# Kernel tuning notes

Measured on AMD Instinct MI355X. Metric: run time of the kernel, lower is better.

## Reference

```python
import jax, jax.numpy as jnp
import numpy as np

B, S, D, H = 4, 2048, 1024, 16
HD = D // H
MASK_VAL = -1e6  # d2l masked_softmax fill value


def setup_inputs() -> dict:
    key = jax.random.key(0)
    ks = jax.random.split(key, 8)
    scale = 1.0 / np.sqrt(D)
    return {
        "queries": jax.random.normal(ks[0], (B, S, D), dtype=jnp.float32),
        "keys": jax.random.normal(ks[1], (B, S, D), dtype=jnp.float32),
        "values": jax.random.normal(ks[2], (B, S, D), dtype=jnp.float32),
        "valid_lens": jax.random.randint(ks[3], (B,), 1, S + 1, dtype=jnp.int32),
        "Wq": jax.random.normal(ks[4], (D, D), dtype=jnp.float32) * scale,
        "Wk": jax.random.normal(ks[5], (D, D), dtype=jnp.float32) * scale,
        "Wv": jax.random.normal(ks[6], (D, D), dtype=jnp.float32) * scale,
        "Wo": jax.random.normal(ks[7], (D, D), dtype=jnp.float32) * scale,
    }


def reference(queries, keys, values, valid_lens, Wq, Wk, Wv, Wo):
    # QKV projections (no bias), then split into heads: [B,S,D] -> [B,H,S,HD]
    def split_heads(x):
        return x.reshape(B, S, H, HD).transpose(0, 2, 1, 3)

    q = split_heads(queries @ Wq)
    k = split_heads(keys @ Wk)
    v = split_heads(values @ Wv)

    # scaled dot-product scores: [B,H,Sq,Sk]
    scores = jnp.einsum('bhqd,bhkd->bhqk', q, k) / jnp.sqrt(jnp.float32(HD))

    # masked softmax over key axis: positions >= valid_len get -1e6 (d2l semantics)
    kv_pos = jnp.arange(S)  # [S]
    mask = kv_pos[None, :] < valid_lens[:, None]  # [B,S]
    scores = jnp.where(mask[:, None, None, :], scores, MASK_VAL)
    attn = jax.nn.softmax(scores, axis=-1)  # dropout=0.0 -> identity

    # weighted sum and merge heads: [B,H,S,HD] -> [B,S,D]
    out = jnp.einsum('bhqk,bhkd->bhqd', attn, v)
    out = out.transpose(0, 2, 1, 3).reshape(B, S, D)
    return out @ Wo
```

## Files before the change

### kernel.cpp

```cpp
#include <hip/hip_runtime.h>
#include <hip/hip_bf16.h>
#include <cstdint>
#include <cstddef>


typedef __hip_bfloat16 bf16;
typedef unsigned short u16;
typedef __attribute__((ext_vector_type(8))) unsigned short ushort8_t;
typedef __attribute__((ext_vector_type(8))) __bf16 bf16x8;
typedef __attribute__((ext_vector_type(4))) float f32x4;

constexpr int Bn = 4, Sn = 2048, Dn = 1024, Hn = 16, HDn = 64;
constexpr size_t BSD = (size_t)Bn * Sn * Dn;
constexpr size_t DD  = (size_t)Dn * Dn;

__device__ __forceinline__ u16 f2b(float f) {
    union { bf16 h; u16 u; } c; c.h = __float2bfloat16(f); return c.u;
}
__device__ __forceinline__ ushort8_t cvt8(float4 a, float4 b) {
    ushort8_t r;
    r[0] = f2b(a.x); r[1] = f2b(a.y); r[2] = f2b(a.z); r[3] = f2b(a.w);
    r[4] = f2b(b.x); r[5] = f2b(b.y); r[6] = f2b(b.z); r[7] = f2b(b.w);
    return r;
}

__global__ __launch_bounds__(256) void transpose_w(
    const float* __restrict__ S0, const float* __restrict__ S1, const float* __restrict__ S2,
    u16* __restrict__ D0, u16* __restrict__ D1, u16* __restrict__ D2)
{
    __shared__ u16 tl[32][33];
    const int z = blockIdx.z;
    const float* S = (z == 0) ? S0 : ((z == 1) ? S1 : S2);
    u16*         D = (z == 0) ? D0 : ((z == 1) ? D1 : D2);
    const int k0 = blockIdx.y * 32, n0 = blockIdx.x * 32;
    const int t = threadIdx.x;
    const int r = t >> 3, c0 = (t & 7) * 4;
    float4 v = *(const float4*)(S + (size_t)(k0 + r) * Dn + n0 + c0);
    tl[r][c0] = f2b(v.x); tl[r][c0 + 1] = f2b(v.y);
    tl[r][c0 + 2] = f2b(v.z); tl[r][c0 + 3] = f2b(v.w);
    __syncthreads();
    ushort4 o;
    o.x = tl[c0][r]; o.y = tl[c0 + 1][r]; o.z = tl[c0 + 2][r]; o.w = tl[c0 + 3][r];
    *(ushort4*)(D + (size_t)(n0 + r) * Dn + k0 + c0) = o;
}

__global__ __launch_bounds__(256) void gemm_qkv(
    const float* __restrict__ A0, const float* __restrict__ A1, const float* __restrict__ A2,
    const u16* __restrict__ B0, const u16* __restrict__ B1, const u16* __restrict__ B2,
    u16* __restrict__ C0, u16* __restrict__ C1, u16* __restrict__ C2, float qscale)
{
    constexpr int K = Dn, BK = 32, BM = 128;
    const int z = blockIdx.z;
    const float* A  = (z == 0) ? A0 : ((z == 1) ? A1 : A2);
    const u16*   Bt = (z == 0) ? B0 : ((z == 1) ? B1 : B2);
    u16*         C  = (z == 0) ? C0 : ((z == 1) ? C1 : C2);
    const float scale = (z == 0) ? qscale : 1.0f;

    __shared__ __attribute__((aligned(16))) u16 As[BM][BK + 8];
    __shared__ __attribute__((aligned(16))) u16 Bs[BM][BK + 8];

    const int t = threadIdx.x, l = t & 63, w = t >> 6;
    const int i = l & 15, j = l >> 4;
    const int row0 = blockIdx.y * BM, col0 = blockIdx.x * BM;
    const int m_off = (w & 1) * 64, n_off = (w >> 1) * 64;
    const int ar = t >> 1, ah = (t & 1) * 16;

    f32x4 acc[4][4] = {};

    for (int k0 = 0; k0 < K; k0 += BK) {
        const float* ap = A + (size_t)(row0 + ar) * K + k0 + ah;
        float4 f0 = *(const float4*)ap,       f1 = *(const float4*)(ap + 4);
        float4 f2 = *(const float4*)(ap + 8), f3 = *(const float4*)(ap + 12);
        const u16* bp = Bt + (size_t)(col0 + ar) * K + k0 + ah;
        ushort8_t bv0 = *(const ushort8_t*)bp, bv1 = *(const ushort8_t*)(bp + 8);
        __syncthreads();
        *(ushort8_t*)&As[ar][ah]     = cvt8(f0, f1);
        *(ushort8_t*)&As[ar][ah + 8] = cvt8(f2, f3);
        *(ushort8_t*)&Bs[ar][ah] = bv0; *(ushort8_t*)&Bs[ar][ah + 8] = bv1;
        __syncthreads();
        bf16x8 af[4], bfr[4];
        #pragma unroll
        for (int mi = 0; mi < 4; mi++)
            af[mi] = *(const bf16x8*)&As[m_off + mi * 16 + i][j * 8];
        #pragma unroll
        for (int ni = 0; ni < 4; ni++)
            bfr[ni] = *(const bf16x8*)&Bs[n_off + ni * 16 + i][j * 8];
        #pragma unroll
        for (int mi = 0; mi < 4; mi++)
            #pragma unroll
            for (int ni = 0; ni < 4; ni++)
                acc[mi][ni] = __builtin_amdgcn_mfma_f32_16x16x32_bf16(
                    af[mi], bfr[ni], acc[mi][ni], 0, 0, 0);
    }

    #pragma unroll
    for (int mi = 0; mi < 4; mi++) {
        #pragma unroll
        for (int r = 0; r < 4; r++) {
            const int m = row0 + m_off + mi * 16 + j * 4 + r;
            const int b = m >> 11, s = m & (Sn - 1);
            #pragma unroll
            for (int ni = 0; ni < 4; ni++) {
                const int n = col0 + n_off + ni * 16 + i;
                const int h = n >> 6, hd = n & (HDn - 1);
                C[(((size_t)(b * Hn + h)) * Sn + s) * HDn + hd] = f2b(acc[mi][ni][r] * scale);
            }
        }
    }
}

__global__ __launch_bounds__(256) void gemm_out(
    const u16* __restrict__ A, const u16* __restrict__ Bt, float* __restrict__ C)
{
    constexpr int K = Dn, BK = 32, BM = 128;
    __shared__ __attribute__((aligned(16))) u16 As[BM][BK + 8];
    __shared__ __attribute__((aligned(16))) u16 Bs[BM][BK + 8];

    const int t = threadIdx.x, l = t & 63, w = t >> 6;
    const int i = l & 15, j = l >> 4;
    const int row0 = blockIdx.y * BM, col0 = blockIdx.x * BM;
    const int m_off = (w & 1) * 64, n_off = (w >> 1) * 64;
    const int ar = t >> 1, ah = (t & 1) * 16;

    f32x4 acc[4][4] = {};

    for (int k0 = 0; k0 < K; k0 += BK) {
        const u16* ap = A  + (size_t)(row0 + ar) * K + k0 + ah;
        const u16* bp = Bt + (size_t)(col0 + ar) * K + k0 + ah;
        ushort8_t av0 = *(const ushort8_t*)ap, av1 = *(const ushort8_t*)(ap + 8);
        ushort8_t bv0 = *(const ushort8_t*)bp, bv1 = *(const ushort8_t*)(bp + 8);
        __syncthreads();
        *(ushort8_t*)&As[ar][ah] = av0; *(ushort8_t*)&As[ar][ah + 8] = av1;
        *(ushort8_t*)&Bs[ar][ah] = bv0; *(ushort8_t*)&Bs[ar][ah + 8] = bv1;
        __syncthreads();
        bf16x8 af[4], bfr[4];
        #pragma unroll
        for (int mi = 0; mi < 4; mi++)
            af[mi] = *(const bf16x8*)&As[m_off + mi * 16 + i][j * 8];
        #pragma unroll
        for (int ni = 0; ni < 4; ni++)
            bfr[ni] = *(const bf16x8*)&Bs[n_off + ni * 16 + i][j * 8];
        #pragma unroll
        for (int mi = 0; mi < 4; mi++)
            #pragma unroll
            for (int ni = 0; ni < 4; ni++)
                acc[mi][ni] = __builtin_amdgcn_mfma_f32_16x16x32_bf16(
                    af[mi], bfr[ni], acc[mi][ni], 0, 0, 0);
    }

    #pragma unroll
    for (int mi = 0; mi < 4; mi++) {
        #pragma unroll
        for (int r = 0; r < 4; r++) {
            const int m = row0 + m_off + mi * 16 + j * 4 + r;
            #pragma unroll
            for (int ni = 0; ni < 4; ni++) {
                const int n = col0 + n_off + ni * 16 + i;
                C[(size_t)m * Dn + n] = acc[mi][ni][r];
            }
        }
    }
}

__global__ __launch_bounds__(512) void attn_mfma(
    const u16* __restrict__ Qh, const u16* __restrict__ Kh, const u16* __restrict__ Vh,
    const int* __restrict__ vlen, u16* __restrict__ Out)
{
    constexpr int TQ = 128, TK = 64;
    __shared__ __attribute__((aligned(16))) u16 Ks[TK][HDn + 8];
    __shared__ __attribute__((aligned(16))) u16 Vt[HDn][TK + 8];
    __shared__ __attribute__((aligned(16))) u16 Ps[TQ][TK + 8];

    const int t = threadIdx.x, l = t & 63, w = t >> 6;
    const int i = l & 15, j = l >> 4;

    const int b    = blockIdx.x & 3;
    const int rest = blockIdx.x >> 2;
    const int h    = rest & 15;
    const int qt   = rest >> 4;
    const int q0   = qt * TQ;
    const int vl   = vlen[b];

    const size_t hoff = ((size_t)(b * Hn + h)) * Sn * HDn;
    const u16* Qg = Qh + hoff + (size_t)q0 * HDn;
    const u16* Kg = Kh + hoff;
    const u16* Vg = Vh + hoff;

    bf16x8 qf[2];
    #pragma unroll
    for (int ks = 0; ks < 2; ks++)
        qf[ks] = *(const bf16x8*)(Qg + (size_t)(w * 16 + i) * HDn + ks * 32 + j * 8);

    f32x4 acc_o[4] = {};
    float l_part[4] = {0.f, 0.f, 0.f, 0.f};

    const int ntiles = (vl + TK - 1) / TK;

    for (int kt = 0; kt < ntiles; kt++) {
        const int ks0 = kt * TK;
        __syncthreads();
        {
            const int kr = t >> 3, kc = (t & 7) * 8;
            *(ushort8_t*)&Ks[kr][kc] =
                *(const ushort8_t*)(Kg + (size_t)(ks0 + kr) * HDn + kc);
        }
        {
            const int vr = (t >> 4) * 2, dc = (t & 15) * 4;
            ushort4 v0 = *(const ushort4*)(Vg + (size_t)(ks0 + vr) * HDn + dc);
            ushort4 v1 = *(const ushort4*)(Vg + (size_t)(ks0 + vr + 1) * HDn + dc);
            *(ushort2*)&Vt[dc + 0][vr] = make_ushort2(v0.x, v1.x);
            *(ushort2*)&Vt[dc + 1][vr] = make_ushort2(v0.y, v1.y);
            *(ushort2*)&Vt[dc + 2][vr] = make_ushort2(v0.z, v1.z);
            *(ushort2*)&Vt[dc + 3][vr] = make_ushort2(v0.w, v1.w);
        }
        __syncthreads();

        f32x4 s[4] = {};
        #pragma unroll
        for (int ks = 0; ks < 2; ks++) {
            bf16x8 kf[4];
            #pragma unroll
            for (int ni = 0; ni < 4; ni++)
                kf[ni] = *(const bf16x8*)&Ks[ni * 16 + i][ks * 32 + j * 8];
            #pragma unroll
            for (int ni = 0; ni < 4; ni++)
                s[ni] = __builtin_amdgcn_mfma_f32_16x16x32_bf16(
                    qf[ks], kf[ni], s[ni], 0, 0, 0);
        }

        const bool tail = (ks0 + TK > vl);
        #pragma unroll
        for (int ni = 0; ni < 4; ni++) {
            const bool keep = !tail || (ks0 + ni * 16 + i < vl);
            #pragma unroll
            for (int r = 0; r < 4; r++) {
                float p = __expf(s[ni][r]);
                p = keep ? p : 0.0f;
                l_part[r] += p;
                Ps[w * 16 + j * 4 + r][ni * 16 + i] = f2b(p);
            }
        }

        #pragma unroll
        for (int ks = 0; ks < 2; ks++) {
            bf16x8 pa = *(const bf16x8*)&Ps[w * 16 + i][ks * 32 + j * 8];
            bf16x8 vb[4];
            #pragma unroll
            for (int di = 0; di < 4; di++)
                vb[di] = *(const bf16x8*)&Vt[di * 16 + i][ks * 32 + j * 8];
            #pragma unroll
            for (int di = 0; di < 4; di++)
                acc_o[di] = __builtin_amdgcn_mfma_f32_16x16x32_bf16(
                    pa, vb[di], acc_o[di], 0, 0, 0);
        }
    }

    #pragma unroll
    for (int r = 0; r < 4; r++) {
        float v = l_part[r];
        #pragma unroll
        for (int d = 1; d < 16; d <<= 1) v += __shfl_xor(v, d, 64);
        l_part[r] = v;
    }

    #pragma unroll
    for (int r = 0; r < 4; r++) {
        const int q = q0 + w * 16 + j * 4 + r;
        const float inv = 1.0f / l_part[r];
        #pragma unroll
        for (int di = 0; di < 4; di++) {
            const int d = di * 16 + i;
            Out[((size_t)b * Sn + q) * Dn + h * HDn + d] = f2b(acc_o[di][r] * inv);
        }
    }
}

extern "C" void kernel_launch(void* const* d_in, const int* in_sizes, int n_in,
                              void* d_out, int out_size, void* d_ws, size_t ws_size,
                              hipStream_t stream)
{
    const float* xq = (const float*)d_in[0];
    const float* xk = (const float*)d_in[1];
    const float* xv = (const float*)d_in[2];
    const int*   vl = (const int*)d_in[3];
    const float* Wq = (const float*)d_in[4];
    const float* Wk = (const float*)d_in[5];
    const float* Wv = (const float*)d_in[6];
    const float* Wo = (const float*)d_in[7];
    float* out = (float*)d_out;

    u16* Qh = (u16*)d_ws;
    u16* Kh = Qh + BSD;
    u16* Vh = Kh + BSD;
    u16* Ao = Vh + BSD;
    u16* WtQ = Ao;
    u16* WtK = WtQ + DD;
    u16* WtV = WtK + DD;
    u16* WoT = Qh;

    transpose_w<<<dim3(32, 32, 3), 256, 0, stream>>>(Wq, Wk, Wv, WtQ, WtK, WtV);
    gemm_qkv<<<dim3(8, 64, 3), 256, 0, stream>>>(xq, xk, xv, WtQ, WtK, WtV,
                                                 Qh, Kh, Vh, 0.125f);
    attn_mfma<<<dim3(Bn * Hn * (Sn / 128)), 512, 0, stream>>>(Qh, Kh, Vh, vl, Ao);
    transpose_w<<<dim3(32, 32, 1), 256, 0, stream>>>(Wo, Wo, Wo, WoT, WoT, WoT);
    gemm_out<<<dim3(8, 64), 256, 0, stream>>>(Ao, WoT, out);
}
```

Baseline: 412.3 us.

## Load GEMM tiles directly into LDS via global_load_lds with swizzle and tile remap

Both projection GEMMs now use the global_load_lds builtin to copy A and B tiles straight from global memory into shared memory, skipping the register round-trip. In the QKV GEMM the A tile is kept as fp32 in LDS with an XOR swizzle, and the bf16 conversion moves to fragment-read time. Block indices are also remapped so that consecutive blocks share row panels, which should improve L2 reuse. The padding on the LDS tiles is dropped, so B-tile fragment reads may suffer bank conflicts, and fp32 staging doubles the LDS footprint for A.

```diff
diff --git a/kernel.cpp b/kernel.cpp
--- a/kernel.cpp
+++ b/kernel.cpp
@@ -17,11 +17,18 @@
 __device__ __forceinline__ u16 f2b(float f) {
     union { bf16 h; u16 u; } c; c.h = __float2bfloat16(f); return c.u;
 }
-__device__ __forceinline__ ushort8_t cvt8(float4 a, float4 b) {
-    ushort8_t r;
-    r[0] = f2b(a.x); r[1] = f2b(a.y); r[2] = f2b(a.z); r[3] = f2b(a.w);
-    r[4] = f2b(b.x); r[5] = f2b(b.y); r[6] = f2b(b.z); r[7] = f2b(b.w);
-    return r;
+
+__device__ __forceinline__ bf16x8 cvt_bf8(f32x4 lo, f32x4 hi) {
+    union { ushort8_t u; bf16x8 b; } c;
+    c.u[0] = f2b(lo[0]); c.u[1] = f2b(lo[1]); c.u[2] = f2b(lo[2]); c.u[3] = f2b(lo[3]);
+    c.u[4] = f2b(hi[0]); c.u[5] = f2b(hi[1]); c.u[6] = f2b(hi[2]); c.u[7] = f2b(hi[3]);
+    return c.b;
+}
+
+__device__ __forceinline__ void gl_lds16(const void* g, void* l) {
+    __builtin_amdgcn_global_load_lds(
+        (const __attribute__((address_space(1))) uint32_t*)g,
+        (__attribute__((address_space(3))) uint32_t*)l, 16, 0, 0);
 }
 
 __global__ __launch_bounds__(256) void transpose_w(
@@ -56,32 +63,45 @@
     u16*         C  = (z == 0) ? C0 : ((z == 1) ? C1 : C2);
     const float scale = (z == 0) ? qscale : 1.0f;
 
-    __shared__ __attribute__((aligned(16))) u16 As[BM][BK + 8];
-    __shared__ __attribute__((aligned(16))) u16 Bs[BM][BK + 8];
+    __shared__ __attribute__((aligned(16))) float As32[BM][BK];
+    __shared__ __attribute__((aligned(16))) u16   Bs[BM][BK];
 
     const int t = threadIdx.x, l = t & 63, w = t >> 6;
     const int i = l & 15, j = l >> 4;
-    const int row0 = blockIdx.y * BM, col0 = blockIdx.x * BM;
+
+    const int wl   = blockIdx.x * 64 + blockIdx.y;
+    const int col0 = (wl & 7) * BM;
+    const int row0 = (wl >> 3) * BM;
     const int m_off = (w & 1) * 64, n_off = (w >> 1) * 64;
-    const int ar = t >> 1, ah = (t & 1) * 16;
+
+    const size_t a_base = (size_t)(row0 + w * 32 + (l >> 3)) * K
+                          + (size_t)(((l & 7) ^ (l >> 3)) * 4);
+    const size_t b_base = (size_t)(col0 + w * 32 + (l >> 2)) * K
+                          + (size_t)((l & 3) * 8);
+    float* a_lds = &As32[w * 32][0];
+    u16*   b_lds = &Bs[w * 32][0];
 
     f32x4 acc[4][4] = {};
 
     for (int k0 = 0; k0 < K; k0 += BK) {
-        const float* ap = A + (size_t)(row0 + ar) * K + k0 + ah;
-        float4 f0 = *(const float4*)ap,       f1 = *(const float4*)(ap + 4);
-        float4 f2 = *(const float4*)(ap + 8), f3 = *(const float4*)(ap + 12);
-        const u16* bp = Bt + (size_t)(col0 + ar) * K + k0 + ah;
-        ushort8_t bv0 = *(const ushort8_t*)bp, bv1 = *(const ushort8_t*)(bp + 8);
-        __syncthreads();
-        *(ushort8_t*)&As[ar][ah]     = cvt8(f0, f1);
-        *(ushort8_t*)&As[ar][ah + 8] = cvt8(f2, f3);
-        *(ushort8_t*)&Bs[ar][ah] = bv0; *(ushort8_t*)&Bs[ar][ah + 8] = bv1;
-        __syncthreads();
+        __syncthreads();
+        #pragma unroll
+        for (int c = 0; c < 4; c++)
+            gl_lds16(A + a_base + (size_t)c * 8 * K + k0, a_lds + c * 8 * BK);
+        #pragma unroll
+        for (int c = 0; c < 2; c++)
+            gl_lds16(Bt + b_base + (size_t)c * 16 * K + k0, b_lds + c * 16 * BK);
+        __syncthreads();
+
         bf16x8 af[4], bfr[4];
-        #pragma unroll
-        for (int mi = 0; mi < 4; mi++)
-            af[mi] = *(const bf16x8*)&As[m_off + mi * 16 + i][j * 8];
+        const int xa = i & 7;
+        #pragma unroll
+        for (int mi = 0; mi < 4; mi++) {
+            const float* rp = &As32[m_off + mi * 16 + i][0];
+            f32x4 lo = *(const f32x4*)(rp + ((2 * j)     ^ xa) * 4);
+            f32x4 hi = *(const f32x4*)(rp + ((2 * j + 1) ^ xa) * 4);
+            af[mi] = cvt_bf8(lo, hi);
+        }
         #pragma unroll
         for (int ni = 0; ni < 4; ni++)
             bfr[ni] = *(const bf16x8*)&Bs[n_off + ni * 16 + i][j * 8];
@@ -113,26 +133,33 @@
     const u16* __restrict__ A, const u16* __restrict__ Bt, float* __restrict__ C)
 {
     constexpr int K = Dn, BK = 32, BM = 128;
-    __shared__ __attribute__((aligned(16))) u16 As[BM][BK + 8];
-    __shared__ __attribute__((aligned(16))) u16 Bs[BM][BK + 8];
+    __shared__ __attribute__((aligned(16))) u16 As[BM][BK];
+    __shared__ __attribute__((aligned(16))) u16 Bs[BM][BK];
 
     const int t = threadIdx.x, l = t & 63, w = t >> 6;
     const int i = l & 15, j = l >> 4;
-    const int row0 = blockIdx.y * BM, col0 = blockIdx.x * BM;
+    const int wl   = blockIdx.x * 64 + blockIdx.y;
+    const int col0 = (wl & 7) * BM;
+    const int row0 = (wl >> 3) * BM;
     const int m_off = (w & 1) * 64, n_off = (w >> 1) * 64;
-    const int ar = t >> 1, ah = (t & 1) * 16;
+
+    const size_t a_base = (size_t)(row0 + w * 32 + (l >> 2)) * K + (size_t)((l & 3) * 8);
+    const size_t b_base = (size_t)(col0 + w * 32 + (l >> 2)) * K + (size_t)((l & 3) * 8);
+    u16* a_lds = &As[w * 32][0];
+    u16* b_lds = &Bs[w * 32][0];
 
     f32x4 acc[4][4] = {};
 
     for (int k0 = 0; k0 < K; k0 += BK) {
-        const u16* ap = A  + (size_t)(row0 + ar) * K + k0 + ah;
-        const u16* bp = Bt + (size_t)(col0 + ar) * K + k0 + ah;
-        ushort8_t av0 = *(const ushort8_t*)ap, av1 = *(const ushort8_t*)(ap + 8);
-        ushort8_t bv0 = *(const ushort8_t*)bp, bv1 = *(const ushort8_t*)(bp + 8);
-        __syncthreads();
-        *(ushort8_t*)&As[ar][ah] = av0; *(ushort8_t*)&As[ar][ah + 8] = av1;
-        *(ushort8_t*)&Bs[ar][ah] = bv0; *(ushort8_t*)&Bs[ar][ah + 8] = bv1;
-        __syncthreads();
+        __syncthreads();
+        #pragma unroll
+        for (int c = 0; c < 2; c++)
+            gl_lds16(A + a_base + (size_t)c * 16 * K + k0, a_lds + c * 16 * BK);
+        #pragma unroll
+        for (int c = 0; c < 2; c++)
+            gl_lds16(Bt + b_base + (size_t)c * 16 * K + k0, b_lds + c * 16 * BK);
+        __syncthreads();
+
         bf16x8 af[4], bfr[4];
         #pragma unroll
         for (int mi = 0; mi < 4; mi++)
```

Result: faster. 386.9 us (-6.2%).
